# Optimization experiments

Hardware: AMD Instinct MI355X
Metric: run time of the kernel (lower is better)

## Reference

```python
import jax, jax.numpy as jnp
import numpy as np

B, D, E, H, C = 2048, 1024, 8, 4096, 1024
TOP_K = 2
LN_EPS = 1e-5


def setup_inputs() -> dict:
    key = jax.random.key(0)
    ks = jax.random.split(key, 5)
    x = jax.random.normal(ks[0], (B, D), dtype=jnp.float32)
    Wr = jax.random.normal(ks[1], (D, E), dtype=jnp.float32) * 0.02
    br = jnp.zeros((E,), dtype=jnp.float32)
    ln_g = jnp.ones((E, D), dtype=jnp.float32)
    ln_b = jnp.zeros((E, D), dtype=jnp.float32)
    W1 = jax.random.normal(ks[2], (E, D, H), dtype=jnp.float32) * 0.02
    b1 = jnp.zeros((E, H), dtype=jnp.float32)
    W2 = jax.random.normal(ks[3], (E, H, C), dtype=jnp.float32) * 0.02
    b2 = jnp.zeros((E, C), dtype=jnp.float32)
    return {"x": x, "Wr": Wr, "br": br, "ln_g": ln_g, "ln_b": ln_b,
            "W1": W1, "b1": b1, "W2": W2, "b2": b2}


def reference(x, Wr, br, ln_g, ln_b, W1, b1, W2, b2):
    # Router (eval mode: no jitter)
    router_logits = x @ Wr + br                       # [B, E]
    topk_vals, topk_idx = jax.lax.top_k(router_logits, TOP_K)
    topk_w = jax.nn.softmax(topk_vals, axis=-1)       # [B, K]
    # Scatter top-k weights into a dense [B, E] combine matrix (indices unique per row)
    w_full = jnp.zeros((x.shape[0], E), dtype=x.dtype)
    w_full = w_full.at[jnp.arange(x.shape[0])[:, None], topk_idx].set(topk_w)
    # Shared LayerNorm statistics, per-expert affine
    mu = jnp.mean(x, axis=-1, keepdims=True)
    var = jnp.mean(jnp.square(x - mu), axis=-1, keepdims=True)
    xn = (x - mu) * jax.lax.rsqrt(var + LN_EPS)       # [B, D]
    xe = xn[:, None, :] * ln_g[None] + ln_b[None]     # [B, E, D]
    # Expert MLPs (dense over experts; combine weights zero-out non-selected experts)
    h = jax.nn.gelu(jnp.einsum('bed,edh->beh', xe, W1) + b1[None], approximate=False)
    y = jnp.einsum('beh,ehc->bec', h, W2) + b2[None]  # [B, E, C]
    out = jnp.einsum('be,bec->bc', w_full, y)         # weighted combine
    return out
```

## Files before the change

kernel.cpp:

```cpp
#include <hip/hip_runtime.h>
#include <hip/hip_bf16.h>

#define B_TOK 2048
#define D_DIM 1024
#define E_NUM 8
#define H_DIM 4096
#define C_DIM 1024
#define CAP   5120
#define MAXT  40

typedef __attribute__((ext_vector_type(8))) short bf16x8;
typedef __attribute__((ext_vector_type(4))) float floatx4;

__device__ __forceinline__ unsigned short f2bf(float f) {
  union { float f; unsigned int u; } a; a.f = f;
  unsigned int u = a.u;
  return (unsigned short)((u + 0x7FFFu + ((u >> 16) & 1u)) >> 16);
}

__device__ __forceinline__ void gload_lds16(const void* g, void* l) {
  __builtin_amdgcn_global_load_lds(
      (const __attribute__((address_space(1))) void*)g,
      (__attribute__((address_space(3))) void*)l, 16, 0, 0);
}

__global__ __launch_bounds__(256) void kinit(float* out_acc, int* slot_tok, int* counts) {
  int id = blockIdx.x * 256 + threadIdx.x;
  out_acc[id] = 0.f;
  if (id < CAP) slot_tok[id] = -1;
  if (id < E_NUM) counts[id] = 0;
}

__global__ __launch_bounds__(256) void krouter(const float* __restrict__ x,
                                               const float* __restrict__ Wr,
                                               const float* __restrict__ br,
                                               int2* meta_i, float4* meta_f, int* counts) {
  int b = blockIdx.x, t = threadIdx.x;
  const float4 xv = *(const float4*)(x + (size_t)b * D_DIM + t * 4);
  float v[10];
  v[0] = xv.x + xv.y + xv.z + xv.w;
  v[1] = xv.x * xv.x + xv.y * xv.y + xv.z * xv.z + xv.w * xv.w;
#pragma unroll
  for (int e = 0; e < 8; e++) v[2 + e] = 0.f;
  const float* wr = Wr + (size_t)(t * 4) * E_NUM;
  float xs[4] = {xv.x, xv.y, xv.z, xv.w};
#pragma unroll
  for (int j = 0; j < 4; j++) {
    float4 wa = *(const float4*)(wr + j * 8);
    float4 wb = *(const float4*)(wr + j * 8 + 4);
    v[2] += xs[j] * wa.x; v[3] += xs[j] * wa.y; v[4] += xs[j] * wa.z; v[5] += xs[j] * wa.w;
    v[6] += xs[j] * wb.x; v[7] += xs[j] * wb.y; v[8] += xs[j] * wb.z; v[9] += xs[j] * wb.w;
  }
#pragma unroll
  for (int i = 0; i < 10; i++) {
    float s = v[i];
#pragma unroll
    for (int off = 32; off > 0; off >>= 1) s += __shfl_down(s, off, 64);
    v[i] = s;
  }
  __shared__ float red[4][10];
  int lane = t & 63, wid = t >> 6;
  if (lane == 0) {
#pragma unroll
    for (int i = 0; i < 10; i++) red[wid][i] = v[i];
  }
  __syncthreads();
  if (t == 0) {
    float f[10];
#pragma unroll
    for (int i = 0; i < 10; i++) f[i] = red[0][i] + red[1][i] + red[2][i] + red[3][i];
    float mu = f[0] * (1.f / 1024.f);
    float var = f[1] * (1.f / 1024.f) - mu * mu;
    float rsig = rsqrtf(var + 1e-5f);
    float lg[8];
#pragma unroll
    for (int e = 0; e < 8; e++) lg[e] = f[2 + e] + br[e];
    int i0 = 0;
#pragma unroll
    for (int e = 1; e < 8; e++) if (lg[e] > lg[i0]) i0 = e;
    int i1 = (i0 == 0) ? 1 : 0;
#pragma unroll
    for (int e = 0; e < 8; e++) if (e != i0 && lg[e] > lg[i1]) i1 = e;
    float ex = expf(lg[i1] - lg[i0]);
    float w0 = 1.f / (1.f + ex);
    float w1 = 1.f - w0;
    atomicAdd(counts + i0, 1);
    atomicAdd(counts + i1, 1);
    meta_i[b] = make_int2(i0, i1);
    meta_f[b] = make_float4(w0, w1, mu, rsig);
  }
}

__global__ void kprefix(const int* counts, int* cursor, int* tmap_e, int* tmap_r) {
  if (threadIdx.x == 0) {
    int total = 0, tt = 0;
    for (int e = 0; e < E_NUM; e++) {
      cursor[e] = total;
      int nt = (counts[e] + 127) >> 7;
      for (int i = 0; i < nt; i++) { tmap_e[tt] = e; tmap_r[tt] = total + i * 128; tt++; }
      total += nt << 7;
    }
    for (; tt < MAXT; tt++) tmap_e[tt] = -1;
  }
}

__global__ __launch_bounds__(256) void kscatter(const float* __restrict__ x,
                                                const float* __restrict__ ln_g,
                                                const float* __restrict__ ln_b,
                                                const int2* __restrict__ meta_i,
                                                const float4* __restrict__ meta_f,
                                                int* cursor, int* slot_tok, float* slot_w,
                                                unsigned short* __restrict__ xe) {
  int b = blockIdx.x, t = threadIdx.x;
  __shared__ int se[2], ss[2];
  __shared__ float smu, srs;
  if (t == 0) {
    int2 mi = meta_i[b];
    float4 mf = meta_f[b];
    int s0 = atomicAdd(cursor + mi.x, 1);
    int s1 = atomicAdd(cursor + mi.y, 1);
    slot_tok[s0] = b; slot_w[s0] = mf.x;
    slot_tok[s1] = b; slot_w[s1] = mf.y;
    se[0] = mi.x; se[1] = mi.y; ss[0] = s0; ss[1] = s1;
    smu = mf.z; srs = mf.w;
  }
  __syncthreads();
  int i = t * 4;
  float4 xv = *(const float4*)(x + (size_t)b * D_DIM + i);
  float mu = smu, rs = srs;
  float xn0 = (xv.x - mu) * rs, xn1 = (xv.y - mu) * rs, xn2 = (xv.z - mu) * rs, xn3 = (xv.w - mu) * rs;
#pragma unroll
  for (int k = 0; k < 2; k++) {
    int e = se[k], s = ss[k];
    float4 g = *(const float4*)(ln_g + (size_t)e * D_DIM + i);
    float4 bb = *(const float4*)(ln_b + (size_t)e * D_DIM + i);
    union { unsigned short us[4]; uint2 v; } u;
    u.us[0] = f2bf(xn0 * g.x + bb.x);
    u.us[1] = f2bf(xn1 * g.y + bb.y);
    u.us[2] = f2bf(xn2 * g.z + bb.z);
    u.us[3] = f2bf(xn3 * g.w + bb.w);
    *(uint2*)(xe + (size_t)s * D_DIM + i) = u.v;
  }
}

__global__ __launch_bounds__(256) void ktranspose(const float* __restrict__ src,
                                                  unsigned short* __restrict__ dst,
                                                  int R, int C) {
  __shared__ float tile[64][65];
  int z = blockIdx.z;
  const float* s = src + (size_t)z * R * C;
  unsigned short* d = dst + (size_t)z * R * C;
  int cx = blockIdx.x * 64, ry = blockIdx.y * 64;
  int t = threadIdx.x;
  int cl4 = (t & 15) * 4, rl = t >> 4;
#pragma unroll
  for (int p = 0; p < 4; p++) {
    int r = rl + p * 16;
    float4 v = *(const float4*)(s + (size_t)(ry + r) * C + cx + cl4);
    tile[r][cl4] = v.x; tile[r][cl4 + 1] = v.y; tile[r][cl4 + 2] = v.z; tile[r][cl4 + 3] = v.w;
  }
  __syncthreads();
#pragma unroll
  for (int p = 0; p < 4; p++) {
    int c = rl + p * 16;
    union { unsigned short us[4]; uint2 v; } u;
    u.us[0] = f2bf(tile[cl4][c]);
    u.us[1] = f2bf(tile[cl4 + 1][c]);
    u.us[2] = f2bf(tile[cl4 + 2][c]);
    u.us[3] = f2bf(tile[cl4 + 3][c]);
    *(uint2*)(d + (size_t)(cx + c) * R + ry + cl4) = u.v;
  }
}

__global__ __launch_bounds__(256) void kgemm1(const unsigned short* __restrict__ xe,
                                              const unsigned short* __restrict__ w1t,
                                              const float* __restrict__ b1,
                                              unsigned short* __restrict__ h,
                                              const int* __restrict__ tmap_e,
                                              const int* __restrict__ tmap_r) {
  int e = tmap_e[blockIdx.y];
  if (e < 0) return;
  int row0 = tmap_r[blockIdx.y];
  int n0 = blockIdx.x * 128;
  const unsigned short* Ab = xe + (size_t)row0 * D_DIM;
  const unsigned short* Bb = w1t + (size_t)e * H_DIM * D_DIM + (size_t)n0 * D_DIM;
  __shared__ unsigned short As[128 * 32];
  __shared__ unsigned short Bs[128 * 32];
  int t = threadIdx.x, lane = t & 63, wid = t >> 6;
  int c0 = wid * 2, c1 = c0 + 1;
  int lr0 = c0 * 16 + (lane >> 2);
  int kc = (lane & 3) * 8;
  const unsigned short* ga0 = Ab + (size_t)lr0 * D_DIM + kc;
  const unsigned short* ga1 = ga0 + 16 * D_DIM;
  const unsigned short* gb0 = Bb + (size_t)lr0 * D_DIM + kc;
  const unsigned short* gb1 = gb0 + 16 * D_DIM;
  unsigned short* la0 = As + c0 * 512;
  unsigned short* la1 = As + c1 * 512;
  unsigned short* lb0 = Bs + c0 * 512;
  unsigned short* lb1 = Bs + c1 * 512;
  int l15 = lane & 15, q = lane >> 4;
  int wm = (wid & 1) * 64, wn = (wid >> 1) * 64;
  const unsigned short* pa[4];
  const unsigned short* pb[4];
#pragma unroll
  for (int i = 0; i < 4; i++) {
    pa[i] = As + (wm + i * 16 + l15) * 32 + q * 8;
    pb[i] = Bs + (wn + i * 16 + l15) * 32 + q * 8;
  }
  floatx4 acc[4][4];
#pragma unroll
  for (int i = 0; i < 4; i++)
#pragma unroll
    for (int j = 0; j < 4; j++) acc[i][j] = (floatx4){0.f, 0.f, 0.f, 0.f};

  for (int k0 = 0; k0 < D_DIM; k0 += 32) {
    gload_lds16(ga0, la0);
    gload_lds16(ga1, la1);
    gload_lds16(gb0, lb0);
    gload_lds16(gb1, lb1);
    __syncthreads();
    bf16x8 af[4], bfr[4];
#pragma unroll
    for (int i = 0; i < 4; i++) { af[i] = *(const bf16x8*)pa[i]; bfr[i] = *(const bf16x8*)pb[i]; }
#pragma unroll
    for (int mt = 0; mt < 4; mt++)
#pragma unroll
      for (int nt = 0; nt < 4; nt++)
        acc[mt][nt] = __builtin_amdgcn_mfma_f32_16x16x32_bf16(af[mt], bfr[nt], acc[mt][nt], 0, 0, 0);
    __syncthreads();
    ga0 += 32; ga1 += 32; gb0 += 32; gb1 += 32;
  }
  float b1v[4];
#pragma unroll
  for (int nt = 0; nt < 4; nt++) b1v[nt] = b1[(size_t)e * H_DIM + n0 + wn + nt * 16 + l15];
#pragma unroll
  for (int mt = 0; mt < 4; mt++) {
    int row = row0 + wm + mt * 16 + q * 4;
#pragma unroll
    for (int nt = 0; nt < 4; nt++) {
      int col = n0 + wn + nt * 16 + l15;
      unsigned short* hp = h + (size_t)row * H_DIM + col;
#pragma unroll
      for (int r = 0; r < 4; r++) {
        float v = acc[mt][nt][r] + b1v[nt];
        v = 0.5f * v * (1.f + erff(v * 0.70710678118f));
        hp[(size_t)r * H_DIM] = f2bf(v);
      }
    }
  }
}

__global__ __launch_bounds__(256) void kgemm2(const unsigned short* __restrict__ h,
                                              const unsigned short* __restrict__ w2t,
                                              const int* __restrict__ slot_tok,
                                              const float* __restrict__ slot_w,
                                              float* __restrict__ out_acc,
                                              const int* __restrict__ tmap_e,
                                              const int* __restrict__ tmap_r) {
  int e = tmap_e[blockIdx.y];
  if (e < 0) return;
  int row0 = tmap_r[blockIdx.y];
  int n0 = blockIdx.x * 128;
  int kz = blockIdx.z;
  const unsigned short* Ab = h + (size_t)row0 * H_DIM + kz * 2048;
  const unsigned short* Bb = w2t + (size_t)e * C_DIM * H_DIM + (size_t)n0 * H_DIM + kz * 2048;
  __shared__ unsigned short As[128 * 32];
  __shared__ unsigned short Bs[128 * 32];
  __shared__ int stok[128];
  __shared__ float swgt[128];
  int t = threadIdx.x, lane = t & 63, wid = t >> 6;
  if (t < 128) { stok[t] = slot_tok[row0 + t]; swgt[t] = slot_w[row0 + t]; }
  int c0 = wid * 2, c1 = c0 + 1;
  int lr0 = c0 * 16 + (lane >> 2);
  int kc = (lane & 3) * 8;
  const unsigned short* ga0 = Ab + (size_t)lr0 * H_DIM + kc;
  const unsigned short* ga1 = ga0 + (size_t)16 * H_DIM;
  const unsigned short* gb0 = Bb + (size_t)lr0 * H_DIM + kc;
  const unsigned short* gb1 = gb0 + (size_t)16 * H_DIM;
  unsigned short* la0 = As + c0 * 512;
  unsigned short* la1 = As + c1 * 512;
  unsigned short* lb0 = Bs + c0 * 512;
  unsigned short* lb1 = Bs + c1 * 512;
  int l15 = lane & 15, q = lane >> 4;
  int wm = (wid & 1) * 64, wn = (wid >> 1) * 64;
  const unsigned short* pa[4];
  const unsigned short* pb[4];
#pragma unroll
  for (int i = 0; i < 4; i++) {
    pa[i] = As + (wm + i * 16 + l15) * 32 + q * 8;
    pb[i] = Bs + (wn + i * 16 + l15) * 32 + q * 8;
  }
  floatx4 acc[4][4];
#pragma unroll
  for (int i = 0; i < 4; i++)
#pragma unroll
    for (int j = 0; j < 4; j++) acc[i][j] = (floatx4){0.f, 0.f, 0.f, 0.f};

  for (int k0 = 0; k0 < 2048; k0 += 32) {
    gload_lds16(ga0, la0);
    gload_lds16(ga1, la1);
    gload_lds16(gb0, lb0);
    gload_lds16(gb1, lb1);
    __syncthreads();
    bf16x8 af[4], bfr[4];
#pragma unroll
    for (int i = 0; i < 4; i++) { af[i] = *(const bf16x8*)pa[i]; bfr[i] = *(const bf16x8*)pb[i]; }
#pragma unroll
    for (int mt = 0; mt < 4; mt++)
#pragma unroll
      for (int nt = 0; nt < 4; nt++)
        acc[mt][nt] = __builtin_amdgcn_mfma_f32_16x16x32_bf16(af[mt], bfr[nt], acc[mt][nt], 0, 0, 0);
    __syncthreads();
    ga0 += 32; ga1 += 32; gb0 += 32; gb1 += 32;
  }
#pragma unroll
  for (int mt = 0; mt < 4; mt++) {
    int rbase = wm + mt * 16 + q * 4;
#pragma unroll
    for (int nt = 0; nt < 4; nt++) {
      int col = n0 + wn + nt * 16 + l15;
#pragma unroll
      for (int r = 0; r < 4; r++) {
        int tk = stok[rbase + r];
        if (tk >= 0)
          atomicAdd(out_acc + (size_t)tk * C_DIM + col, swgt[rbase + r] * acc[mt][nt][r]);
      }
    }
  }
}

__global__ __launch_bounds__(256) void kfinal(const float* __restrict__ out_acc,
                                              const int2* __restrict__ meta_i,
                                              const float4* __restrict__ meta_f,
                                              const float* __restrict__ b2,
                                              float* __restrict__ out) {
  int b = blockIdx.x, t = threadIdx.x;
  int i = t * 4;
  int2 mi = meta_i[b];
  float4 mf = meta_f[b];
  float4 a = *(const float4*)(out_acc + (size_t)b * C_DIM + i);
  float4 p = *(const float4*)(b2 + (size_t)mi.x * C_DIM + i);
  float4 qv = *(const float4*)(b2 + (size_t)mi.y * C_DIM + i);
  float4 o;
  o.x = a.x + mf.x * p.x + mf.y * qv.x;
  o.y = a.y + mf.x * p.y + mf.y * qv.y;
  o.z = a.z + mf.x * p.z + mf.y * qv.z;
  o.w = a.w + mf.x * p.w + mf.y * qv.w;
  *(float4*)(out + (size_t)b * C_DIM + i) = o;
}

extern "C" void kernel_launch(void* const* d_in, const int* in_sizes, int n_in,
                              void* d_out, int out_size, void* d_ws, size_t ws_size,
                              hipStream_t stream) {
  const float* x    = (const float*)d_in[0];
  const float* Wr   = (const float*)d_in[1];
  const float* br   = (const float*)d_in[2];
  const float* ln_g = (const float*)d_in[3];
  const float* ln_b = (const float*)d_in[4];
  const float* W1   = (const float*)d_in[5];
  const float* b1   = (const float*)d_in[6];
  const float* W2   = (const float*)d_in[7];
  const float* b2   = (const float*)d_in[8];

  char* w = (char*)d_ws;
  auto alloc = [&](size_t sz) { char* p = w; w += (sz + 255) & ~(size_t)255; return p; };
  unsigned short* W1t = (unsigned short*)alloc((size_t)E_NUM * H_DIM * D_DIM * 2);
  unsigned short* W2t = (unsigned short*)alloc((size_t)E_NUM * C_DIM * H_DIM * 2);
  unsigned short* xe  = (unsigned short*)alloc((size_t)CAP * D_DIM * 2);
  unsigned short* hb  = (unsigned short*)alloc((size_t)CAP * H_DIM * 2);
  float* out_acc      = (float*)alloc((size_t)B_TOK * C_DIM * 4);
  int2* meta_i        = (int2*)alloc((size_t)B_TOK * 8);
  float4* meta_f      = (float4*)alloc((size_t)B_TOK * 16);
  int* counts         = (int*)alloc(64);
  int* cursor         = (int*)alloc(64);
  int* tmap_e         = (int*)alloc(MAXT * 4);
  int* tmap_r         = (int*)alloc(MAXT * 4);
  int* slot_tok       = (int*)alloc(CAP * 4);
  float* slot_w       = (float*)alloc(CAP * 4);

  hipLaunchKernelGGL(ktranspose, dim3(H_DIM / 64, D_DIM / 64, E_NUM), dim3(256), 0, stream,
                     W1, W1t, D_DIM, H_DIM);
  hipLaunchKernelGGL(ktranspose, dim3(C_DIM / 64, H_DIM / 64, E_NUM), dim3(256), 0, stream,
                     W2, W2t, H_DIM, C_DIM);
  hipLaunchKernelGGL(kinit, dim3(B_TOK * C_DIM / 256), dim3(256), 0, stream,
                     out_acc, slot_tok, counts);
  hipLaunchKernelGGL(krouter, dim3(B_TOK), dim3(256), 0, stream,
                     x, Wr, br, meta_i, meta_f, counts);
  hipLaunchKernelGGL(kprefix, dim3(1), dim3(64), 0, stream,
                     counts, cursor, tmap_e, tmap_r);
  hipLaunchKernelGGL(kscatter, dim3(B_TOK), dim3(256), 0, stream,
                     x, ln_g, ln_b, meta_i, meta_f, cursor, slot_tok, slot_w, xe);
  hipLaunchKernelGGL(kgemm1, dim3(H_DIM / 128, MAXT), dim3(256), 0, stream,
                     xe, W1t, b1, hb, tmap_e, tmap_r);
  hipLaunchKernelGGL(kgemm2, dim3(C_DIM / 128, MAXT, 2), dim3(256), 0, stream,
                     hb, W2t, slot_tok, slot_w, out_acc, tmap_e, tmap_r);
  hipLaunchKernelGGL(kfinal, dim3(B_TOK), dim3(256), 0, stream,
                     out_acc, meta_i, meta_f, b2, (float*)d_out);
}
```

Baseline: 577.8 us.

## Double-buffer LDS, swizzle layout, remap blocks across XCDs, split GEMM2 K four ways

Both expert GEMMs now use two LDS buffers, so the global-to-LDS load of the next K tile overlaps the MFMA work on the current one. LDS columns are XOR-swizzled to cut bank conflicts on fragment reads. Block indices are remapped so consecutive hardware blocks are spread across the 8 XCDs, each XCD getting a contiguous slice of tiles for L2 reuse. GEMM2 splits K four ways instead of two, which adds parallelism but doubles the atomic adds into the output.

```diff
diff --git a/kernel.cpp b/kernel.cpp
--- a/kernel.cpp
+++ b/kernel.cpp
@@ -178,34 +178,34 @@
                                               unsigned short* __restrict__ h,
                                               const int* __restrict__ tmap_e,
                                               const int* __restrict__ tmap_r) {
-  int e = tmap_e[blockIdx.y];
+  int orig = blockIdx.y * 32 + blockIdx.x;
+  int s = (orig & 7) * 160 + (orig >> 3);
+  int bx = s & 31, by = s >> 5;
+  int e = tmap_e[by];
   if (e < 0) return;
-  int row0 = tmap_r[blockIdx.y];
-  int n0 = blockIdx.x * 128;
+  int row0 = tmap_r[by];
+  int n0 = bx * 128;
   const unsigned short* Ab = xe + (size_t)row0 * D_DIM;
   const unsigned short* Bb = w1t + (size_t)e * H_DIM * D_DIM + (size_t)n0 * D_DIM;
-  __shared__ unsigned short As[128 * 32];
-  __shared__ unsigned short Bs[128 * 32];
+  __shared__ unsigned short As[2][128 * 32];
+  __shared__ unsigned short Bs[2][128 * 32];
   int t = threadIdx.x, lane = t & 63, wid = t >> 6;
   int c0 = wid * 2, c1 = c0 + 1;
-  int lr0 = c0 * 16 + (lane >> 2);
-  int kc = (lane & 3) * 8;
-  const unsigned short* ga0 = Ab + (size_t)lr0 * D_DIM + kc;
+  int lr = lane >> 2;
+  int kc = ((lane & 3) ^ ((lane >> 3) & 3)) * 8;
+  const unsigned short* ga0 = Ab + (size_t)(c0 * 16 + lr) * D_DIM + kc;
   const unsigned short* ga1 = ga0 + 16 * D_DIM;
-  const unsigned short* gb0 = Bb + (size_t)lr0 * D_DIM + kc;
+  const unsigned short* gb0 = Bb + (size_t)(c0 * 16 + lr) * D_DIM + kc;
   const unsigned short* gb1 = gb0 + 16 * D_DIM;
-  unsigned short* la0 = As + c0 * 512;
-  unsigned short* la1 = As + c1 * 512;
-  unsigned short* lb0 = Bs + c0 * 512;
-  unsigned short* lb1 = Bs + c1 * 512;
   int l15 = lane & 15, q = lane >> 4;
   int wm = (wid & 1) * 64, wn = (wid >> 1) * 64;
-  const unsigned short* pa[4];
-  const unsigned short* pb[4];
+  int offA[4], offB[4];
 #pragma unroll
   for (int i = 0; i < 4; i++) {
-    pa[i] = As + (wm + i * 16 + l15) * 32 + q * 8;
-    pb[i] = Bs + (wn + i * 16 + l15) * 32 + q * 8;
+    int ra = wm + i * 16 + l15;
+    int rb = wn + i * 16 + l15;
+    offA[i] = ra * 32 + ((q ^ ((ra >> 1) & 3)) * 8);
+    offB[i] = rb * 32 + ((q ^ ((rb >> 1) & 3)) * 8);
   }
   floatx4 acc[4][4];
 #pragma unroll
@@ -213,23 +213,45 @@
 #pragma unroll
     for (int j = 0; j < 4; j++) acc[i][j] = (floatx4){0.f, 0.f, 0.f, 0.f};
 
-  for (int k0 = 0; k0 < D_DIM; k0 += 32) {
-    gload_lds16(ga0, la0);
-    gload_lds16(ga1, la1);
-    gload_lds16(gb0, lb0);
-    gload_lds16(gb1, lb1);
+#define G1_STAGE(bsel)                              \
+  do {                                              \
+    gload_lds16(ga0, &As[bsel][c0 * 512]);          \
+    gload_lds16(ga1, &As[bsel][c1 * 512]);          \
+    gload_lds16(gb0, &Bs[bsel][c0 * 512]);          \
+    gload_lds16(gb1, &Bs[bsel][c1 * 512]);          \
+    ga0 += 32; ga1 += 32; gb0 += 32; gb1 += 32;     \
+  } while (0)
+
+#define G1_COMPUTE(bsel)                                                    \
+  do {                                                                      \
+    bf16x8 af[4], bfr[4];                                                   \
+    _Pragma("unroll") for (int i = 0; i < 4; i++) {                         \
+      af[i] = *(const bf16x8*)(&As[bsel][offA[i]]);                         \
+      bfr[i] = *(const bf16x8*)(&Bs[bsel][offB[i]]);                        \
+    }                                                                       \
+    _Pragma("unroll") for (int mt = 0; mt < 4; mt++)                        \
+      _Pragma("unroll") for (int nt = 0; nt < 4; nt++)                      \
+        acc[mt][nt] = __builtin_amdgcn_mfma_f32_16x16x32_bf16(af[mt], bfr[nt], acc[mt][nt], 0, 0, 0); \
+  } while (0)
+
+  G1_STAGE(0);
+  __syncthreads();
+#pragma unroll 1
+  for (int it = 0; it < D_DIM / 64 - 1; it++) {
+    G1_STAGE(1);
+    G1_COMPUTE(0);
     __syncthreads();
-    bf16x8 af[4], bfr[4];
-#pragma unroll
-    for (int i = 0; i < 4; i++) { af[i] = *(const bf16x8*)pa[i]; bfr[i] = *(const bf16x8*)pb[i]; }
-#pragma unroll
-    for (int mt = 0; mt < 4; mt++)
-#pragma unroll
-      for (int nt = 0; nt < 4; nt++)
-        acc[mt][nt] = __builtin_amdgcn_mfma_f32_16x16x32_bf16(af[mt], bfr[nt], acc[mt][nt], 0, 0, 0);
+    G1_STAGE(0);
+    G1_COMPUTE(1);
     __syncthreads();
-    ga0 += 32; ga1 += 32; gb0 += 32; gb1 += 32;
-  }
+  }
+  G1_STAGE(1);
+  G1_COMPUTE(0);
+  __syncthreads();
+  G1_COMPUTE(1);
+#undef G1_STAGE
+#undef G1_COMPUTE
+
   float b1v[4];
 #pragma unroll
   for (int nt = 0; nt < 4; nt++) b1v[nt] = b1[(size_t)e * H_DIM + n0 + wn + nt * 16 + l15];
@@ -257,38 +279,40 @@
                                               float* __restrict__ out_acc,
                                               const int* __restrict__ tmap_e,
                                               const int* __restrict__ tmap_r) {
-  int e = tmap_e[blockIdx.y];
+  int orig = (blockIdx.z * MAXT + blockIdx.y) * 8 + blockIdx.x;
+  int s = (orig & 7) * 160 + (orig >> 3);
+  int bx = s & 7;
+  int rest = s >> 3;
+  int by = rest % MAXT;
+  int kz = rest / MAXT;
+  int e = tmap_e[by];
   if (e < 0) return;
-  int row0 = tmap_r[blockIdx.y];
-  int n0 = blockIdx.x * 128;
-  int kz = blockIdx.z;
-  const unsigned short* Ab = h + (size_t)row0 * H_DIM + kz * 2048;
-  const unsigned short* Bb = w2t + (size_t)e * C_DIM * H_DIM + (size_t)n0 * H_DIM + kz * 2048;
-  __shared__ unsigned short As[128 * 32];
-  __shared__ unsigned short Bs[128 * 32];
+  int row0 = tmap_r[by];
+  int n0 = bx * 128;
+  const unsigned short* Ab = h + (size_t)row0 * H_DIM + kz * 1024;
+  const unsigned short* Bb = w2t + (size_t)e * C_DIM * H_DIM + (size_t)n0 * H_DIM + kz * 1024;
+  __shared__ unsigned short As[2][128 * 32];
+  __shared__ unsigned short Bs[2][128 * 32];
   __shared__ int stok[128];
   __shared__ float swgt[128];
   int t = threadIdx.x, lane = t & 63, wid = t >> 6;
   if (t < 128) { stok[t] = slot_tok[row0 + t]; swgt[t] = slot_w[row0 + t]; }
   int c0 = wid * 2, c1 = c0 + 1;
-  int lr0 = c0 * 16 + (lane >> 2);
-  int kc = (lane & 3) * 8;
-  const unsigned short* ga0 = Ab + (size_t)lr0 * H_DIM + kc;
+  int lr = lane >> 2;
+  int kc = ((lane & 3) ^ ((lane >> 3) & 3)) * 8;
+  const unsigned short* ga0 = Ab + (size_t)(c0 * 16 + lr) * H_DIM + kc;
   const unsigned short* ga1 = ga0 + (size_t)16 * H_DIM;
-  const unsigned short* gb0 = Bb + (size_t)lr0 * H_DIM + kc;
+  const unsigned short* gb0 = Bb + (size_t)(c0 * 16 + lr) * H_DIM + kc;
   const unsigned short* gb1 = gb0 + (size_t)16 * H_DIM;
-  unsigned short* la0 = As + c0 * 512;
-  unsigned short* la1 = As + c1 * 512;
-  unsigned short* lb0 = Bs + c0 * 512;
-  unsigned short* lb1 = Bs + c1 * 512;
   int l15 = lane & 15, q = lane >> 4;
   int wm = (wid & 1) * 64, wn = (wid >> 1) * 64;
-  const unsigned short* pa[4];
-  const unsigned short* pb[4];
+  int offA[4], offB[4];
 #pragma unroll
   for (int i = 0; i < 4; i++) {
-    pa[i] = As + (wm + i * 16 + l15) * 32 + q * 8;
-    pb[i] = Bs + (wn + i * 16 + l15) * 32 + q * 8;
+    int ra = wm + i * 16 + l15;
+    int rb = wn + i * 16 + l15;
+    offA[i] = ra * 32 + ((q ^ ((ra >> 1) & 3)) * 8);
+    offB[i] = rb * 32 + ((q ^ ((rb >> 1) & 3)) * 8);
   }
   floatx4 acc[4][4];
 #pragma unroll
@@ -296,23 +320,45 @@
 #pragma unroll
     for (int j = 0; j < 4; j++) acc[i][j] = (floatx4){0.f, 0.f, 0.f, 0.f};
 
-  for (int k0 = 0; k0 < 2048; k0 += 32) {
-    gload_lds16(ga0, la0);
-    gload_lds16(ga1, la1);
-    gload_lds16(gb0, lb0);
-    gload_lds16(gb1, lb1);
+#define G2_STAGE(bsel)                              \
+  do {                                              \
+    gload_lds16(ga0, &As[bsel][c0 * 512]);          \
+    gload_lds16(ga1, &As[bsel][c1 * 512]);          \
+    gload_lds16(gb0, &Bs[bsel][c0 * 512]);          \
+    gload_lds16(gb1, &Bs[bsel][c1 * 512]);          \
+    ga0 += 32; ga1 += 32; gb0 += 32; gb1 += 32;     \
+  } while (0)
+
+#define G2_COMPUTE(bsel)                                                    \
+  do {                                                                      \
+    bf16x8 af[4], bfr[4];                                                   \
+    _Pragma("unroll") for (int i = 0; i < 4; i++) {                         \
+      af[i] = *(const bf16x8*)(&As[bsel][offA[i]]);                         \
+      bfr[i] = *(const bf16x8*)(&Bs[bsel][offB[i]]);                        \
+    }                                                                       \
+    _Pragma("unroll") for (int mt = 0; mt < 4; mt++)                        \
+      _Pragma("unroll") for (int nt = 0; nt < 4; nt++)                      \
+        acc[mt][nt] = __builtin_amdgcn_mfma_f32_16x16x32_bf16(af[mt], bfr[nt], acc[mt][nt], 0, 0, 0); \
+  } while (0)
+
+  G2_STAGE(0);
+  __syncthreads();
+#pragma unroll 1
+  for (int it = 0; it < 1024 / 64 - 1; it++) {
+    G2_STAGE(1);
+    G2_COMPUTE(0);
     __syncthreads();
-    bf16x8 af[4], bfr[4];
-#pragma unroll
-    for (int i = 0; i < 4; i++) { af[i] = *(const bf16x8*)pa[i]; bfr[i] = *(const bf16x8*)pb[i]; }
-#pragma unroll
-    for (int mt = 0; mt < 4; mt++)
-#pragma unroll
-      for (int nt = 0; nt < 4; nt++)
-        acc[mt][nt] = __builtin_amdgcn_mfma_f32_16x16x32_bf16(af[mt], bfr[nt], acc[mt][nt], 0, 0, 0);
+    G2_STAGE(0);
+    G2_COMPUTE(1);
     __syncthreads();
-    ga0 += 32; ga1 += 32; gb0 += 32; gb1 += 32;
-  }
+  }
+  G2_STAGE(1);
+  G2_COMPUTE(0);
+  __syncthreads();
+  G2_COMPUTE(1);
+#undef G2_STAGE
+#undef G2_COMPUTE
+
 #pragma unroll
   for (int mt = 0; mt < 4; mt++) {
     int rbase = wm + mt * 16 + q * 4;
@@ -392,7 +438,7 @@
                      x, ln_g, ln_b, meta_i, meta_f, cursor, slot_tok, slot_w, xe);
   hipLaunchKernelGGL(kgemm1, dim3(H_DIM / 128, MAXT), dim3(256), 0, stream,
                      xe, W1t, b1, hb, tmap_e, tmap_r);
-  hipLaunchKernelGGL(kgemm2, dim3(C_DIM / 128, MAXT, 2), dim3(256), 0, stream,
+  hipLaunchKernelGGL(kgemm2, dim3(C_DIM / 128, MAXT, 4), dim3(256), 0, stream,
                      hb, W2t, slot_tok, slot_w, out_acc, tmap_e, tmap_r);
   hipLaunchKernelGGL(kfinal, dim3(B_TOK), dim3(256), 0, stream,
                      out_acc, meta_i, meta_f, b2, (float*)d_out);
```

Result: slower. 602.9 us (+4.3%).
